# Performance work log

Measured on AMD Instinct MI355X. Metric: run time of the kernel, lower is better.

Reference implementation:

```python
import jax, jax.numpy as jnp
import numpy as np

H = 8          # n_heads
M = 16         # max_dist
U = 512        # n_units
DH = U // H    # d_head
EPS = 1e-3     # keras LayerNormalization default epsilon
NEG = -2.0**32 + 1.0


def _rel_table(pe, T):
    # pe: [2M+1, DH]; returns [T, T, DH] with rel[i, j] = pe[clip(j - i, -M, M) + M]
    i = jnp.arange(T)
    idx = jnp.clip(i[None, :] - i[:, None], -M, M) + M
    return pe[idx]


def _split_heads(x):
    # [B, T, U] -> [H*B, T, DH]  (head-major, matching tf.concat(tf.split(x, H, 2), 0))
    B, T, _ = x.shape
    return x.reshape(B, T, H, DH).transpose(2, 0, 1, 3).reshape(H * B, T, DH)


def _merge_heads(x, B):
    # [H*B, T, DH] -> [B, T, U]
    T = x.shape[1]
    return x.reshape(H, B, T, DH).transpose(1, 2, 0, 3).reshape(B, T, U)


def setup_inputs() -> dict:
    key = jax.random.key(0)
    ks = jax.random.split(key, 10)
    B, T = 8, 1024
    s = 1.0 / np.sqrt(U)
    inp = {
        'q': jax.random.normal(ks[0], (B, T, U), jnp.float32),
        'k': jax.random.normal(ks[1], (B, T, U), jnp.float32),
        'v': jax.random.normal(ks[2], (B, T, U), jnp.float32),
        'Wq': jax.random.normal(ks[3], (U, U), jnp.float32) * s,
        'bq': jnp.zeros((U,), jnp.float32),
        'Wk': jax.random.normal(ks[4], (U, U), jnp.float32) * s,
        'bk': jnp.zeros((U,), jnp.float32),
        'Wv': jax.random.normal(ks[5], (U, U), jnp.float32) * s,
        'bv': jnp.zeros((U,), jnp.float32),
        'Wo': jax.random.normal(ks[6], (U, U), jnp.float32) * s,
        'bo': jnp.zeros((U,), jnp.float32),
        'gamma': jnp.ones((U,), jnp.float32),
        'beta': jnp.zeros((U,), jnp.float32),
        'pe_k': jax.random.normal(ks[7], (2 * M + 1, DH), jnp.float32) * 0.05,
        'pe_v': jax.random.normal(ks[8], (2 * M + 1, DH), jnp.float32) * 0.05,
    }
    return inp


def reference(q, k, v, Wq, bq, Wk, bk, Wv, bv, Wo, bo, gamma, beta, pe_k, pe_v):
    B, T, _ = q.shape
    relu = jax.nn.relu
    q_emb = relu(q @ Wq + bq)
    k_emb = relu(k @ Wk + bk)
    v_emb = relu(v @ Wv + bv)
    qh = _split_heads(q_emb)   # [HB, T, DH]
    kh = _split_heads(k_emb)
    vh = _split_heads(v_emb)

    attn = jnp.einsum('btd,bsd->bts', qh, kh)
    rel_k = _rel_table(pe_k, T)                       # [T, T, DH]
    attn = attn + jnp.einsum('btd,tsd->bts', qh, rel_k)
    attn = attn / jnp.asarray(DH, attn.dtype) ** 0.5

    causal = jnp.tril(jnp.ones((T, T), jnp.bool_))
    attn = jnp.where(causal[None], attn, jnp.asarray(NEG, attn.dtype))
    w = jax.nn.softmax(attn, axis=-1)

    out = jnp.einsum('bts,bsd->btd', w, vh)
    rel_v = _rel_table(pe_v, T)
    out = out + jnp.einsum('bts,tsd->btd', w, rel_v)

    out = _merge_heads(out, B)                        # [B, T, U]
    out = relu(out @ Wo + bo)
    out = out + q

    mu = jnp.mean(out, axis=-1, keepdims=True)
    var = jnp.mean(jnp.square(out - mu), axis=-1, keepdims=True)
    return (out - mu) * jax.lax.rsqrt(var + EPS) * gamma + beta
```

## Files before the change

### kernel.cpp

```cpp
#include <hip/hip_runtime.h>
#include <hip/hip_bf16.h>

#define T_SEQ 1024
#define U_DIM 512
#define LN_EPS 1e-3f

typedef float  f32x4  __attribute__((ext_vector_type(4)));
typedef short  bf16x8 __attribute__((ext_vector_type(8)));

__device__ __forceinline__ unsigned short f2bf(float f) {
    union { float f; unsigned u; } x; x.f = f;
    unsigned r = x.u + 0x7fffu + ((x.u >> 16) & 1u);
    return (unsigned short)(r >> 16);
}
__device__ __forceinline__ float b2f(short s) {
    union { unsigned u; float f; } x; x.u = ((unsigned)(unsigned short)s) << 16;
    return x.f;
}
__device__ __forceinline__ int packbf(float a, float b) {
    return (int)((unsigned)f2bf(a) | ((unsigned)f2bf(b) << 16));
}
__device__ __forceinline__ void async_copy16(void* lds, const void* g) {
    __builtin_amdgcn_global_load_lds((const __attribute__((address_space(1))) void*)g,
                                     (__attribute__((address_space(3))) void*)lds, 16, 0, 0);
}

__global__ __launch_bounds__(256) void prep_wt(
        const float* __restrict__ Wq, const float* __restrict__ Wk,
        const float* __restrict__ Wv, const float* __restrict__ Wo,
        short* __restrict__ wt) {
    __shared__ float Ws[64][65];
    const int bid = blockIdx.x, t = threadIdx.x;
    const int z = bid >> 6, tile = bid & 63;
    const float* W = (z == 0) ? Wq : (z == 1) ? Wk : (z == 2) ? Wv : Wo;
    short* Wt = wt + (size_t)z * 262144;
    const int k0 = (tile >> 3) * 64, n0 = (tile & 7) * 64;
    {
        const int kr = t >> 2, cs = (t & 3) * 16;
        const float4* src = (const float4*)(W + (size_t)(k0 + kr) * 512 + n0 + cs);
#pragma unroll
        for (int i = 0; i < 4; ++i) {
            float4 vv = src[i];
            Ws[kr][cs + 4 * i + 0] = vv.x;
            Ws[kr][cs + 4 * i + 1] = vv.y;
            Ws[kr][cs + 4 * i + 2] = vv.z;
            Ws[kr][cs + 4 * i + 3] = vv.w;
        }
    }
    __syncthreads();
    {
        const int nr = t >> 2, ks = (t & 3) * 16;
        int4 w0, w1;
        w0.x = packbf(Ws[ks + 0][nr], Ws[ks + 1][nr]);
        w0.y = packbf(Ws[ks + 2][nr], Ws[ks + 3][nr]);
        w0.z = packbf(Ws[ks + 4][nr], Ws[ks + 5][nr]);
        w0.w = packbf(Ws[ks + 6][nr], Ws[ks + 7][nr]);
        w1.x = packbf(Ws[ks + 8][nr], Ws[ks + 9][nr]);
        w1.y = packbf(Ws[ks + 10][nr], Ws[ks + 11][nr]);
        w1.z = packbf(Ws[ks + 12][nr], Ws[ks + 13][nr]);
        w1.w = packbf(Ws[ks + 14][nr], Ws[ks + 15][nr]);
        short* dst = Wt + (size_t)(n0 + nr) * 512 + k0 + ks;
        *(int4*)dst = w0;
        *(int4*)(dst + 8) = w1;
    }
}

template <int AFP32, int OUT>
__global__ __launch_bounds__(256) void gemm_mfma(
        const void* __restrict__ A0, const void* __restrict__ A1, const void* __restrict__ A2,
        const short* __restrict__ Wt0, const short* __restrict__ Wt1, const short* __restrict__ Wt2,
        const float* __restrict__ b0p, const float* __restrict__ b1p, const float* __restrict__ b2p,
        const float* __restrict__ resid,
        void* __restrict__ O0, void* __restrict__ O1, void* __restrict__ O2) {
    __shared__ short As[2 * 8192];
    __shared__ short Bs[2 * 8192];

    const int z = blockIdx.z;
    const void* Av = (z == 0) ? A0 : (z == 1) ? A1 : A2;
    const short* Wz = (z == 0) ? Wt0 : (z == 1) ? Wt1 : Wt2;
    const float* bz = (z == 0) ? b0p : (z == 1) ? b1p : b2p;
    void* Ov = (z == 0) ? O0 : (z == 1) ? O1 : O2;

    const int tid = threadIdx.x;
    const int m0 = blockIdx.x * 128, n0 = blockIdx.y * 128;
    const int w = tid >> 6, lane = tid & 63;
    const int n15 = lane & 15, g = lane >> 4;
    const int mh = w >> 1, nh = w & 1;
    const int am = tid >> 1, akh = tid & 1;

    f32x4 acc[4][4];
#pragma unroll
    for (int i = 0; i < 4; ++i)
#pragma unroll
        for (int j = 0; j < 4; ++j) acc[i][j] = (f32x4){0.f, 0.f, 0.f, 0.f};

    float4 areg[8];

#define LOAD_A(CK)                                                                       \
    do {                                                                                 \
        const float* asrc = (const float*)Av + (size_t)(m0 + am) * 512 + (CK) * 64 + akh * 32; \
        _Pragma("unroll")                                                                \
        for (int i = 0; i < 8; ++i) areg[i] = ((const float4*)asrc)[i];                  \
    } while (0)

#define STORE_A(BUF)                                                                     \
    do {                                                                                 \
        short* cell = As + (BUF) * 8192 + (akh * 8 + (am >> 4)) * 512;                   \
        _Pragma("unroll")                                                                \
        for (int gg = 0; gg < 4; ++gg) {                                                 \
            int4 wv;                                                                     \
            wv.x = packbf(areg[2 * gg].x, areg[2 * gg].y);                               \
            wv.y = packbf(areg[2 * gg].z, areg[2 * gg].w);                               \
            wv.z = packbf(areg[2 * gg + 1].x, areg[2 * gg + 1].y);                       \
            wv.w = packbf(areg[2 * gg + 1].z, areg[2 * gg + 1].w);                       \
            *(int4*)(cell + ((am & 15) + 16 * gg) * 8) = wv;                             \
        }                                                                                \
    } while (0)

#define STAGE_B(CK, BUF)                                                                 \
    do {                                                                                 \
        if (w < 2) {                                                                     \
            _Pragma("unroll")                                                            \
            for (int i = 0; i < 8; ++i) {                                                \
                const int kc = i >> 2, nt = w * 4 + (i & 3);                             \
                const short* gp = Wz + (size_t)(n0 + nt * 16 + n15) * 512 + (CK) * 64 + kc * 32 + g * 8; \
                async_copy16(Bs + (BUF) * 8192 + (kc * 8 + nt) * 512, gp);               \
            }                                                                            \
        }                                                                                \
    } while (0)

#define STAGE_A_ASYNC(CK, BUF)                                                           \
    do {                                                                                 \
        if (w >= 2) {                                                                    \
            _Pragma("unroll")                                                            \
            for (int i = 0; i < 8; ++i) {                                                \
                const int kc = i >> 2, mt = (w - 2) * 4 + (i & 3);                       \
                const short* gp = (const short*)Av + (size_t)(m0 + mt * 16 + n15) * 512 + (CK) * 64 + kc * 32 + g * 8; \
                async_copy16(As + (BUF) * 8192 + (kc * 8 + mt) * 512, gp);               \
            }                                                                            \
        }                                                                                \
    } while (0)

    if (AFP32) {
        LOAD_A(0);
        STORE_A(0);
        STAGE_B(0, 0);
        LOAD_A(1);
    } else {
        STAGE_B(0, 0);
        STAGE_A_ASYNC(0, 0);
    }

    for (int ck = 0; ck < 8; ++ck) {
        const int cb = ck & 1, nb = cb ^ 1;
        __syncthreads();
        if (ck < 7) {
            STAGE_B(ck + 1, nb);
            if (!AFP32) STAGE_A_ASYNC(ck + 1, nb);
        }
#pragma unroll
        for (int kc = 0; kc < 2; ++kc) {
            bf16x8 af[4], bfv[4];
#pragma unroll
            for (int i = 0; i < 4; ++i)
                af[i] = *(const bf16x8*)(As + cb * 8192 + (kc * 8 + mh * 4 + i) * 512 + lane * 8);
#pragma unroll
            for (int j = 0; j < 4; ++j)
                bfv[j] = *(const bf16x8*)(Bs + cb * 8192 + (kc * 8 + nh * 4 + j) * 512 + lane * 8);
#pragma unroll
            for (int i = 0; i < 4; ++i)
#pragma unroll
                for (int j = 0; j < 4; ++j)
                    acc[i][j] = __builtin_amdgcn_mfma_f32_16x16x32_bf16(af[i], bfv[j], acc[i][j], 0, 0, 0);
        }
        if (AFP32 && ck < 7) {
            STORE_A(nb);
            if (ck < 6) LOAD_A(ck + 2);
        }
    }
#undef LOAD_A
#undef STORE_A
#undef STAGE_B
#undef STAGE_A_ASYNC

    const int mbase = m0 + mh * 64 + g * 4;
    const int nbase = n0 + nh * 64 + n15;
    const bool even = (n15 & 1) == 0;
    float bj[4];
#pragma unroll
    for (int j = 0; j < 4; ++j) bj[j] = bz[nbase + j * 16];

#pragma unroll
    for (int i = 0; i < 4; ++i) {
        const int mrow = mbase + i * 16;
#pragma unroll
        for (int j = 0; j < 4; ++j) {
            const int ncol = nbase + j * 16;
            f32x4 a = acc[i][j];
            float v0 = fmaxf(a[0] + bj[j], 0.f);
            float v1 = fmaxf(a[1] + bj[j], 0.f);
            float v2 = fmaxf(a[2] + bj[j], 0.f);
            float v3 = fmaxf(a[3] + bj[j], 0.f);
            if (OUT == 0) {
                unsigned t01 = (unsigned)packbf(v0, v1);
                unsigned t23 = (unsigned)packbf(v2, v3);
                unsigned x01 = (unsigned)__shfl_xor((int)t01, 1, 64);
                unsigned x23 = (unsigned)__shfl_xor((int)t23, 1, 64);
                short* Oz = (short*)Ov;
                if (even) {
                    unsigned d0 = (t01 & 0xffffu) | (x01 << 16);
                    unsigned d1 = (t01 >> 16) | (x01 & 0xffff0000u);
                    *(unsigned*)(Oz + (size_t)(mrow + 0) * 512 + ncol) = d0;
                    *(unsigned*)(Oz + (size_t)(mrow + 1) * 512 + ncol) = d1;
                } else {
                    unsigned d2 = (x23 & 0xffffu) | (t23 << 16);
                    unsigned d3 = (x23 >> 16) | (t23 & 0xffff0000u);
                    *(unsigned*)(Oz + (size_t)(mrow + 2) * 512 + ncol - 1) = d2;
                    *(unsigned*)(Oz + (size_t)(mrow + 3) * 512 + ncol - 1) = d3;
                }
            } else {
                float x0 = __shfl_xor(v0, 1, 64);
                float x1 = __shfl_xor(v1, 1, 64);
                float x2 = __shfl_xor(v2, 1, 64);
                float x3 = __shfl_xor(v3, 1, 64);
                float* Oz = (float*)Ov;
                if (even) {
                    float2 r0 = *(const float2*)(resid + (size_t)(mrow + 0) * 512 + ncol);
                    float2 r1 = *(const float2*)(resid + (size_t)(mrow + 1) * 512 + ncol);
                    *(float2*)(Oz + (size_t)(mrow + 0) * 512 + ncol) = make_float2(v0 + r0.x, x0 + r0.y);
                    *(float2*)(Oz + (size_t)(mrow + 1) * 512 + ncol) = make_float2(v1 + r1.x, x1 + r1.y);
                } else {
                    float2 r2 = *(const float2*)(resid + (size_t)(mrow + 2) * 512 + ncol - 1);
                    float2 r3 = *(const float2*)(resid + (size_t)(mrow + 3) * 512 + ncol - 1);
                    *(float2*)(Oz + (size_t)(mrow + 2) * 512 + ncol - 1) = make_float2(x2 + r2.x, v2 + r2.y);
                    *(float2*)(Oz + (size_t)(mrow + 3) * 512 + ncol - 1) = make_float2(x3 + r3.x, v3 + r3.y);
                }
            }
        }
    }
}

__global__ __launch_bounds__(256) void attn_mfma(
        const short* __restrict__ qe, const short* __restrict__ ke,
        const short* __restrict__ ve, const float* __restrict__ pe_k,
        float* __restrict__ ml, short* __restrict__ ao) {
    __shared__ short Kc[2 * 4096];
    __shared__ short Vc[2 * 4096];
    __shared__ float qpeS[4 * 16 * 17];

    const int tid = threadIdx.x;
    const int bx = blockIdx.x;
    const int hb = blockIdx.y;
    const int h = hb >> 3, b = hb & 7;
    const int w = tid >> 6, lane = tid & 63;
    const int g = lane >> 4, n15 = lane & 15;
    const int sp = tid & 31, dbase = (tid >> 5) * 8;
    const int tA = bx;
    float* qpeW = qpeS + w * (16 * 17);

    const size_t rowbase = (size_t)b * T_SEQ;

    int qn = 0;
    bf16x8 Bq[2];
    float qpe0 = 0.f;
    float m_r = -3.0e38f, l_r = 0.f;
    f32x4 oacc[4];

#define SETUP(TILE)                                                                      \
    do {                                                                                 \
        qn = (TILE) * 64 + w * 16;                                                       \
        _Pragma("unroll")                                                                \
        for (int kh = 0; kh < 2; ++kh)                                                   \
            Bq[kh] = *(const bf16x8*)(qe + (rowbase + qn + n15) * U_DIM + h * 64 + kh * 32 + g * 8); \
        f32x4 qa[2];                                                                     \
        qa[0] = (f32x4){0.f, 0.f, 0.f, 0.f};                                             \
        qa[1] = (f32x4){0.f, 0.f, 0.f, 0.f};                                             \
        _Pragma("unroll")                                                                \
        for (int mt = 0; mt < 2; ++mt)                                                   \
        _Pragma("unroll")                                                                \
        for (int kh = 0; kh < 2; ++kh) {                                                 \
            const float* src = pe_k + (mt * 16 + n15) * 64 + kh * 32 + g * 8;            \
            float4 f0 = *(const float4*)src;                                             \
            float4 f1 = *(const float4*)(src + 4);                                       \
            bf16x8 fr;                                                                   \
            fr[0] = (short)f2bf(f0.x); fr[1] = (short)f2bf(f0.y);                        \
            fr[2] = (short)f2bf(f0.z); fr[3] = (short)f2bf(f0.w);                        \
            fr[4] = (short)f2bf(f1.x); fr[5] = (short)f2bf(f1.y);                        \
            fr[6] = (short)f2bf(f1.z); fr[7] = (short)f2bf(f1.w);                        \
            qa[mt] = __builtin_amdgcn_mfma_f32_16x16x32_bf16(fr, Bq[kh], qa[mt], 0, 0, 0); \
        }                                                                                \
        _Pragma("unroll")                                                                \
        for (int mt = 0; mt < 2; ++mt)                                                   \
        _Pragma("unroll")                                                                \
        for (int r = 0; r < 4; ++r) {                                                    \
            const int ri = mt * 16 + 4 * g + r;                                          \
            if (ri <= 16) qpeW[n15 * 17 + ri] = qa[mt][r];                               \
        }                                                                                \
        qpe0 = qpeW[n15 * 17];                                                           \
        m_r = -3.0e38f; l_r = 0.f;                                                       \
        _Pragma("unroll")                                                                \
        for (int dt = 0; dt < 4; ++dt) oacc[dt] = (f32x4){0.f, 0.f, 0.f, 0.f};           \
    } while (0)

#define STAGE_K(S, BUF)                                                                  \
    do {                                                                                 \
        _Pragma("unroll")                                                                \
        for (int j = 0; j < 2; ++j) {                                                    \
            const int cc = w * 2 + j, kh = cc >> 2, mt = cc & 3;                         \
            const short* gp = ke + (rowbase + (S) + mt * 16 + n15) * U_DIM + h * 64 + kh * 32 + g * 8; \
            async_copy16(Kc + (BUF) * 4096 + cc * 512, gp);                              \
        }                                                                                \
    } while (0)

#define LOAD_V(S)                                                                        \
    do {                                                                                 \
        const short* r0 = ve + (rowbase + (S) + 2 * sp) * U_DIM + h * 64 + dbase;        \
        vx = *(const bf16x8*)r0;                                                         \
        vy = *(const bf16x8*)(r0 + U_DIM);                                               \
    } while (0)

#define STORE_V(BUF)                                                                     \
    do {                                                                                 \
        const int vkh = sp >> 4, vg = (sp & 15) >> 2, vj = (sp & 3) * 2;                 \
        _Pragma("unroll")                                                                \
        for (int i = 0; i < 8; ++i) {                                                    \
            const int d = dbase + i;                                                     \
            int pv = (int)((unsigned short)vx[i]) | (((int)(unsigned short)vy[i]) << 16);\
            *(int*)(Vc + (BUF) * 4096 + (vkh * 4 + (d >> 4)) * 512 + ((d & 15) + 16 * vg) * 8 + vj) = pv; \
        }                                                                                \
    } while (0)

    SETUP(tA);
    bf16x8 vx, vy;
    STAGE_K(0, 0);
    LOAD_V(0);
    STORE_V(0);

    for (int gs = 0; gs <= 16; ++gs) {
        const int cb = gs & 1, nb = cb ^ 1;
        const int s0 = (gs <= tA) ? gs * 64 : (gs - tA - 1) * 64;
        __syncthreads();
        if (gs < 16) {
            const int sn = (gs + 1 <= tA) ? (gs + 1) * 64 : (gs - tA) * 64;
            STAGE_K(sn, nb);
            LOAD_V(sn);
        }

        {
            int cls[4];
#pragma unroll
            for (int mt = 0; mt < 4; ++mt) {
                const int slo = s0 + mt * 16;
                cls[mt] = (slo > qn + 15) ? 0 : ((slo + 31 < qn) ? 1 : 2);
            }
            f32x4 c[4];
#pragma unroll
            for (int mt = 0; mt < 4; ++mt) c[mt] = (f32x4){0.f, 0.f, 0.f, 0.f};
#pragma unroll
            for (int mt = 0; mt < 4; ++mt) {
                if (!cls[mt]) continue;
#pragma unroll
                for (int kh = 0; kh < 2; ++kh) {
                    bf16x8 ak = *(const bf16x8*)(Kc + cb * 4096 + (kh * 4 + mt) * 512 + lane * 8);
                    c[mt] = __builtin_amdgcn_mfma_f32_16x16x32_bf16(ak, Bq[kh], c[mt], 0, 0, 0);
                }
            }

            const int qg = qn + n15;
            float sc[4][4];
            float pmax = -3.0e38f;
#pragma unroll
            for (int mt = 0; mt < 4; ++mt) {
                if (cls[mt] == 0) {
#pragma unroll
                    for (int r = 0; r < 4; ++r) sc[mt][r] = -3.0e38f;
                } else if (cls[mt] == 1) {
#pragma unroll
                    for (int r = 0; r < 4; ++r) {
                        sc[mt][r] = (c[mt][r] + qpe0) * 0.125f;
                        pmax = fmaxf(pmax, sc[mt][r]);
                    }
                } else {
#pragma unroll
                    for (int r = 0; r < 4; ++r) {
                        const int sg = s0 + mt * 16 + 4 * g + r;
                        const int dlt = sg - qg;
                        if (dlt <= 0) {
                            const int ri = (dlt < -16) ? 0 : (dlt + 16);
                            sc[mt][r] = (c[mt][r] + qpeW[n15 * 17 + ri]) * 0.125f;
                            pmax = fmaxf(pmax, sc[mt][r]);
                        } else {
                            sc[mt][r] = -3.0e38f;
                        }
                    }
                }
            }
            pmax = fmaxf(pmax, __shfl_xor(pmax, 16, 64));
            pmax = fmaxf(pmax, __shfl_xor(pmax, 32, 64));
            const float mnew = fmaxf(m_r, pmax);
            const float alpha = __expf(m_r - mnew);
            float p[4][4];
            float psum = 0.f;
#pragma unroll
            for (int mt = 0; mt < 4; ++mt)
#pragma unroll
            for (int r = 0; r < 4; ++r) {
                const float pv = (cls[mt] == 0) ? 0.f : __expf(sc[mt][r] - mnew);
                p[mt][r] = pv;
                psum += pv;
            }
            psum += __shfl_xor(psum, 16, 64);
            psum += __shfl_xor(psum, 32, 64);
            l_r = l_r * alpha + psum;
            m_r = mnew;

            int pk01[4], pk23[4];
#pragma unroll
            for (int mt = 0; mt < 4; ++mt) {
                pk01[mt] = packbf(p[mt][0], p[mt][1]);
                pk23[mt] = packbf(p[mt][2], p[mt][3]);
            }
            const int srcA = ((g & 1) * 2) * 16 + n15;
            const int srcB = srcA + 16;
            const bool selHi = (g >> 1) != 0;
            float aO[4];
#pragma unroll
            for (int r = 0; r < 4; ++r) aO[r] = __shfl(alpha, 4 * g + r, 64);
#pragma unroll
            for (int dt = 0; dt < 4; ++dt)
#pragma unroll
            for (int r = 0; r < 4; ++r) oacc[dt][r] *= aO[r];
#pragma unroll
            for (int kh = 0; kh < 2; ++kh) {
                if (cls[2 * kh] == 0 && cls[2 * kh + 1] == 0) continue;
                const int a0l = __shfl(pk01[2 * kh], srcA, 64);
                const int a0h = __shfl(pk01[2 * kh + 1], srcA, 64);
                const int a1l = __shfl(pk23[2 * kh], srcA, 64);
                const int a1h = __shfl(pk23[2 * kh + 1], srcA, 64);
                const int a2l = __shfl(pk01[2 * kh], srcB, 64);
                const int a2h = __shfl(pk01[2 * kh + 1], srcB, 64);
                const int a3l = __shfl(pk23[2 * kh], srcB, 64);
                const int a3h = __shfl(pk23[2 * kh + 1], srcB, 64);
                union { int i[4]; bf16x8 v; } au;
                au.i[0] = selHi ? a0h : a0l;
                au.i[1] = selHi ? a1h : a1l;
                au.i[2] = selHi ? a2h : a2l;
                au.i[3] = selHi ? a3h : a3l;
#pragma unroll
                for (int dt = 0; dt < 4; ++dt) {
                    bf16x8 bv = *(const bf16x8*)(Vc + cb * 4096 + (kh * 4 + dt) * 512 + lane * 8);
                    oacc[dt] = __builtin_amdgcn_mfma_f32_16x16x32_bf16(au.v, bv, oacc[dt], 0, 0, 0);
                }
            }
        }

        if (gs == tA) {
            if (g == 0)
                *(float2*)(ml + ((size_t)hb * T_SEQ + qn + n15) * 2) = make_float2(m_r, l_r);
#pragma unroll
            for (int r = 0; r < 4; ++r) {
                const float lq = __shfl(l_r, 4 * g + r, 64);
                const float linv = 1.0f / lq;
                short* dst = ao + (rowbase + qn + 4 * g + r) * U_DIM + h * 64 + n15;
#pragma unroll
                for (int dt = 0; dt < 4; ++dt)
                    dst[dt * 16] = (short)f2bf(oacc[dt][r] * linv);
            }
            SETUP(15 - bx);
        }

        if (gs < 16) STORE_V(nb);
    }

    if (g == 0)
        *(float2*)(ml + ((size_t)hb * T_SEQ + qn + n15) * 2) = make_float2(m_r, l_r);
#pragma unroll
    for (int r = 0; r < 4; ++r) {
        const float lq = __shfl(l_r, 4 * g + r, 64);
        const float linv = 1.0f / lq;
        short* dst = ao + (rowbase + qn + 4 * g + r) * U_DIM + h * 64 + n15;
#pragma unroll
        for (int dt = 0; dt < 4; ++dt)
            dst[dt * 16] = (short)f2bf(oacc[dt][r] * linv);
    }
#undef SETUP
#undef STAGE_K
#undef LOAD_V
#undef STORE_V
}

__global__ __launch_bounds__(256) void band_relv(
        const short* __restrict__ qe, const short* __restrict__ ke,
        const float* __restrict__ pe_k, const float* __restrict__ pe_v,
        const float* __restrict__ ml, short* __restrict__ ao) {
    __shared__ float pek[17 * 64];
    __shared__ float pev[17 * 64];
    const int tb = blockIdx.x, hb = blockIdx.y;
    const int h = hb >> 3, b = hb & 7;
    const int tid = threadIdx.x;
    for (int i = tid; i < 17 * 64; i += 256) {
        pek[i] = b2f((short)f2bf(pe_k[i]));
        pev[i] = pe_v[i];
    }
    __syncthreads();

    const int t = tb * 64 + (tid >> 2);
    const int p = (tid & 3) * 16;
    const short* qp = qe + (size_t)(b * T_SEQ + t) * U_DIM + h * 64 + p;
    bf16x8 qa = *(const bf16x8*)qp, qb2 = *(const bf16x8*)(qp + 8);
    float qv[16];
#pragma unroll
    for (int i = 0; i < 8; ++i) { qv[i] = b2f(qa[i]); qv[8 + i] = b2f(qb2[i]); }

    float dots[17];
#pragma unroll
    for (int ri = 0; ri < 17; ++ri) {
        const int s = t - 16 + ri;
        float acc = 0.f;
        if (s >= 0) {
            const short* kp = ke + (size_t)(b * T_SEQ + s) * U_DIM + h * 64 + p;
            bf16x8 ka = *(const bf16x8*)kp, kb2 = *(const bf16x8*)(kp + 8);
#pragma unroll
            for (int d = 0; d < 8; ++d) {
                acc += qv[d] * b2f(ka[d]);
                acc += qv[8 + d] * b2f(kb2[d]);
            }
#pragma unroll
            for (int d = 0; d < 16; ++d) acc += qv[d] * pek[ri * 64 + p + d];
        }
        dots[ri] = acc;
    }
#pragma unroll
    for (int ri = 0; ri < 17; ++ri) {
        dots[ri] += __shfl_xor(dots[ri], 1, 64);
        dots[ri] += __shfl_xor(dots[ri], 2, 64);
    }

    const float2 mlv = *(const float2*)(ml + ((size_t)hb * T_SEQ + t) * 2);
    const float m = mlv.x, linv = 1.0f / mlv.y;
    float wv[17];
    float wsum = 0.f;
#pragma unroll
    for (int ri = 0; ri < 17; ++ri) {
        const int s = t - 16 + ri;
        const float wr = (s >= 0) ? __expf(dots[ri] * 0.125f - m) * linv : 0.f;
        wv[ri] = wr;
        wsum += wr;
    }
    wv[0] += 1.0f - wsum;

    float relv[16];
#pragma unroll
    for (int d = 0; d < 16; ++d) relv[d] = 0.f;
#pragma unroll
    for (int ri = 0; ri < 17; ++ri)
#pragma unroll
        for (int d = 0; d < 16; ++d) relv[d] += wv[ri] * pev[ri * 64 + p + d];

    short* op = ao + (size_t)(b * T_SEQ + t) * U_DIM + h * 64 + p;
    bf16x8 a0 = *(const bf16x8*)op, a1 = *(const bf16x8*)(op + 8);
    int4 o0, o1;
    o0.x = packbf(b2f(a0[0]) + relv[0],  b2f(a0[1]) + relv[1]);
    o0.y = packbf(b2f(a0[2]) + relv[2],  b2f(a0[3]) + relv[3]);
    o0.z = packbf(b2f(a0[4]) + relv[4],  b2f(a0[5]) + relv[5]);
    o0.w = packbf(b2f(a0[6]) + relv[6],  b2f(a0[7]) + relv[7]);
    o1.x = packbf(b2f(a1[0]) + relv[8],  b2f(a1[1]) + relv[9]);
    o1.y = packbf(b2f(a1[2]) + relv[10], b2f(a1[3]) + relv[11]);
    o1.z = packbf(b2f(a1[4]) + relv[12], b2f(a1[5]) + relv[13]);
    o1.w = packbf(b2f(a1[6]) + relv[14], b2f(a1[7]) + relv[15]);
    *(int4*)op = o0;
    *(int4*)(op + 8) = o1;
}

__global__ __launch_bounds__(256) void ln_kernel(float* __restrict__ io,
                                                 const float* __restrict__ gamma,
                                                 const float* __restrict__ beta) {
    const int row = blockIdx.x * 4 + (threadIdx.x >> 6);
    const int lane = threadIdx.x & 63;
    float* rp = io + (size_t)row * 512 + lane * 8;
    float4 a = *(const float4*)rp;
    float4 c = *(const float4*)(rp + 4);
    float v[8] = {a.x, a.y, a.z, a.w, c.x, c.y, c.z, c.w};

    float s = v[0] + v[1] + v[2] + v[3] + v[4] + v[5] + v[6] + v[7];
#pragma unroll
    for (int off = 1; off < 64; off <<= 1) s += __shfl_xor(s, off, 64);
    const float mu = s * (1.0f / 512.0f);

    float sq = 0.f;
#pragma unroll
    for (int i = 0; i < 8; ++i) { v[i] -= mu; sq += v[i] * v[i]; }
#pragma unroll
    for (int off = 1; off < 64; off <<= 1) sq += __shfl_xor(sq, off, 64);
    const float rs = rsqrtf(sq * (1.0f / 512.0f) + LN_EPS);

    const float4 g0 = *(const float4*)(gamma + lane * 8);
    const float4 g1 = *(const float4*)(gamma + lane * 8 + 4);
    const float4 b0 = *(const float4*)(beta + lane * 8);
    const float4 b1 = *(const float4*)(beta + lane * 8 + 4);
    float4 o0, o1;
    o0.x = v[0] * rs * g0.x + b0.x;
    o0.y = v[1] * rs * g0.y + b0.y;
    o0.z = v[2] * rs * g0.z + b0.z;
    o0.w = v[3] * rs * g0.w + b0.w;
    o1.x = v[4] * rs * g1.x + b1.x;
    o1.y = v[5] * rs * g1.y + b1.y;
    o1.z = v[6] * rs * g1.z + b1.z;
    o1.w = v[7] * rs * g1.w + b1.w;
    *(float4*)rp = o0;
    *(float4*)(rp + 4) = o1;
}

extern "C" void kernel_launch(void* const* d_in, const int* in_sizes, int n_in,
                              void* d_out, int out_size, void* d_ws, size_t ws_size,
                              hipStream_t stream) {
    const float* q     = (const float*)d_in[0];
    const float* k     = (const float*)d_in[1];
    const float* v     = (const float*)d_in[2];
    const float* Wq    = (const float*)d_in[3];
    const float* bq    = (const float*)d_in[4];
    const float* Wk    = (const float*)d_in[5];
    const float* bk    = (const float*)d_in[6];
    const float* Wv    = (const float*)d_in[7];
    const float* bv    = (const float*)d_in[8];
    const float* Wo    = (const float*)d_in[9];
    const float* bo    = (const float*)d_in[10];
    const float* gamma = (const float*)d_in[11];
    const float* beta  = (const float*)d_in[12];
    const float* pe_k  = (const float*)d_in[13];
    const float* pe_v  = (const float*)d_in[14];
    float* out = (float*)d_out;

    char* base = (char*)d_ws;
    short* qe = (short*)(base);
    short* ke = (short*)(base + (((size_t)8) << 20));
    short* ve = (short*)(base + (((size_t)16) << 20));
    short* ao = (short*)(base + (((size_t)24) << 20));
    short* wt = (short*)(base + (((size_t)32) << 20));
    float* ml = (float*)(base + (((size_t)34) << 20));
    short* wtq = wt, *wtk = wt + 262144, *wtv = wt + 2 * 262144, *wto = wt + 3 * 262144;

    prep_wt<<<dim3(256), 256, 0, stream>>>(Wq, Wk, Wv, Wo, wt);
    gemm_mfma<1, 0><<<dim3(64, 4, 3), 256, 0, stream>>>(
        q, k, v, wtq, wtk, wtv, bq, bk, bv, nullptr, qe, ke, ve);
    attn_mfma<<<dim3(8, 64), 256, 0, stream>>>(qe, ke, ve, pe_k, ml, ao);
    band_relv<<<dim3(16, 64), 256, 0, stream>>>(qe, ke, pe_k, pe_v, ml, ao);
    gemm_mfma<0, 1><<<dim3(64, 4, 1), 256, 0, stream>>>(
        ao, ao, ao, wto, wto, wto, bo, bo, bo, q, out, out, out);
    ln_kernel<<<dim3(2048), 256, 0, stream>>>(out, gamma, beta);
}
```

Measured before the change: 264.3 us.

## Split attention work per query tile, coalesce fp32 A loads, shrink output GEMM tile

After: 240.2 us. 1.1x faster.

```diff
diff --git a/kernel.cpp b/kernel.cpp
--- a/kernel.cpp
+++ b/kernel.cpp
@@ -65,14 +65,18 @@
     }
 }
 
-template <int AFP32, int OUT>
+template <int AFP32, int OUT, int BM>
 __global__ __launch_bounds__(256) void gemm_mfma(
         const void* __restrict__ A0, const void* __restrict__ A1, const void* __restrict__ A2,
         const short* __restrict__ Wt0, const short* __restrict__ Wt1, const short* __restrict__ Wt2,
         const float* __restrict__ b0p, const float* __restrict__ b1p, const float* __restrict__ b2p,
         const float* __restrict__ resid,
         void* __restrict__ O0, void* __restrict__ O1, void* __restrict__ O2) {
-    __shared__ short As[2 * 8192];
+    constexpr int ASZ = BM * 64;
+    constexpr int NW  = (BM == 128) ? 2 : 4;
+    constexpr int AJ  = 8 / NW;
+    constexpr int ACB = BM / 32;
+    __shared__ short As[2 * ASZ];
     __shared__ short Bs[2 * 8192];
 
     const int z = blockIdx.z;
@@ -82,38 +86,37 @@
     void* Ov = (z == 0) ? O0 : (z == 1) ? O1 : O2;
 
     const int tid = threadIdx.x;
-    const int m0 = blockIdx.x * 128, n0 = blockIdx.y * 128;
+    const int m0 = blockIdx.x * BM, n0 = blockIdx.y * 128;
     const int w = tid >> 6, lane = tid & 63;
     const int n15 = lane & 15, g = lane >> 4;
-    const int mh = w >> 1, nh = w & 1;
-    const int am = tid >> 1, akh = tid & 1;
-
-    f32x4 acc[4][4];
+    const int mh = w / NW, nh = w % NW;
+    const int lr = tid >> 4, c4 = tid & 15;
+
+    f32x4 acc[4][AJ];
 #pragma unroll
     for (int i = 0; i < 4; ++i)
 #pragma unroll
-        for (int j = 0; j < 4; ++j) acc[i][j] = (f32x4){0.f, 0.f, 0.f, 0.f};
+        for (int j = 0; j < AJ; ++j) acc[i][j] = (f32x4){0.f, 0.f, 0.f, 0.f};
 
     float4 areg[8];
 
 #define LOAD_A(CK)                                                                       \
     do {                                                                                 \
-        const float* asrc = (const float*)Av + (size_t)(m0 + am) * 512 + (CK) * 64 + akh * 32; \
-        _Pragma("unroll")                                                                \
-        for (int i = 0; i < 8; ++i) areg[i] = ((const float4*)asrc)[i];                  \
+        const float* abase = (const float*)Av + (size_t)(m0 + lr) * 512 + (CK) * 64 + c4 * 4; \
+        _Pragma("unroll")                                                                \
+        for (int i = 0; i < 8; ++i) areg[i] = *(const float4*)(abase + (size_t)8192 * i); \
     } while (0)
 
 #define STORE_A(BUF)                                                                     \
     do {                                                                                 \
-        short* cell = As + (BUF) * 8192 + (akh * 8 + (am >> 4)) * 512;                   \
-        _Pragma("unroll")                                                                \
-        for (int gg = 0; gg < 4; ++gg) {                                                 \
-            int4 wv;                                                                     \
-            wv.x = packbf(areg[2 * gg].x, areg[2 * gg].y);                               \
-            wv.y = packbf(areg[2 * gg].z, areg[2 * gg].w);                               \
-            wv.z = packbf(areg[2 * gg + 1].x, areg[2 * gg + 1].y);                       \
-            wv.w = packbf(areg[2 * gg + 1].z, areg[2 * gg + 1].w);                       \
-            *(int4*)(cell + ((am & 15) + 16 * gg) * 8) = wv;                             \
+        short* sb = As + (BUF) * ASZ + ((c4 >> 3) * (BM / 16)) * 512 + lr * 8 +          \
+                    ((c4 & 7) >> 1) * 128 + (c4 & 1) * 4;                                \
+        _Pragma("unroll")                                                                \
+        for (int i = 0; i < 8; ++i) {                                                    \
+            int2 wv;                                                                     \
+            wv.x = packbf(areg[i].x, areg[i].y);                                         \
+            wv.y = packbf(areg[i].z, areg[i].w);                                         \
+            *(int2*)(sb + i * 512) = wv;                                                 \
         }                                                                                \
     } while (0)
 
@@ -133,10 +136,10 @@
     do {                                                                                 \
         if (w >= 2) {                                                                    \
             _Pragma("unroll")                                                            \
-            for (int i = 0; i < 8; ++i) {                                                \
-                const int kc = i >> 2, mt = (w - 2) * 4 + (i & 3);                       \
+            for (int i = 0; i < 2 * ACB; ++i) {                                          \
+                const int kc = i / ACB, mt = (w - 2) * ACB + (i % ACB);                  \
                 const short* gp = (const short*)Av + (size_t)(m0 + mt * 16 + n15) * 512 + (CK) * 64 + kc * 32 + g * 8; \
-                async_copy16(As + (BUF) * 8192 + (kc * 8 + mt) * 512, gp);               \
+                async_copy16(As + (BUF) * ASZ + (kc * (BM / 16) + mt) * 512, gp);        \
             }                                                                            \
         }                                                                                \
     } while (0)
@@ -160,17 +163,17 @@
         }
 #pragma unroll
         for (int kc = 0; kc < 2; ++kc) {
-            bf16x8 af[4], bfv[4];
+            bf16x8 af[4], bfv[AJ];
 #pragma unroll
             for (int i = 0; i < 4; ++i)
-                af[i] = *(const bf16x8*)(As + cb * 8192 + (kc * 8 + mh * 4 + i) * 512 + lane * 8);
-#pragma unroll
-            for (int j = 0; j < 4; ++j)
-                bfv[j] = *(const bf16x8*)(Bs + cb * 8192 + (kc * 8 + nh * 4 + j) * 512 + lane * 8);
+                af[i] = *(const bf16x8*)(As + cb * ASZ + (kc * (BM / 16) + mh * 4 + i) * 512 + lane * 8);
+#pragma unroll
+            for (int j = 0; j < AJ; ++j)
+                bfv[j] = *(const bf16x8*)(Bs + cb * 8192 + (kc * 8 + nh * AJ + j) * 512 + lane * 8);
 #pragma unroll
             for (int i = 0; i < 4; ++i)
 #pragma unroll
-                for (int j = 0; j < 4; ++j)
+                for (int j = 0; j < AJ; ++j)
                     acc[i][j] = __builtin_amdgcn_mfma_f32_16x16x32_bf16(af[i], bfv[j], acc[i][j], 0, 0, 0);
         }
         if (AFP32 && ck < 7) {
@@ -184,17 +187,17 @@
 #undef STAGE_A_ASYNC
 
     const int mbase = m0 + mh * 64 + g * 4;
-    const int nbase = n0 + nh * 64 + n15;
+    const int nbase = n0 + nh * (AJ * 16) + n15;
     const bool even = (n15 & 1) == 0;
-    float bj[4];
-#pragma unroll
-    for (int j = 0; j < 4; ++j) bj[j] = bz[nbase + j * 16];
+    float bj[AJ];
+#pragma unroll
+    for (int j = 0; j < AJ; ++j) bj[j] = bz[nbase + j * 16];
 
 #pragma unroll
     for (int i = 0; i < 4; ++i) {
         const int mrow = mbase + i * 16;
 #pragma unroll
-        for (int j = 0; j < 4; ++j) {
+        for (int j = 0; j < AJ; ++j) {
             const int ncol = nbase + j * 16;
             f32x4 a = acc[i][j];
             float v0 = fmaxf(a[0] + bj[j], 0.f);
@@ -249,13 +252,14 @@
     __shared__ float qpeS[4 * 16 * 17];
 
     const int tid = threadIdx.x;
-    const int bx = blockIdx.x;
-    const int hb = blockIdx.y;
+    const int bid = blockIdx.x;
+    const int rank = (bid & 3) + 4 * (bid >> 8);
+    const int hb = (bid >> 2) & 63;
+    const int tt = 15 - rank;
     const int h = hb >> 3, b = hb & 7;
     const int w = tid >> 6, lane = tid & 63;
     const int g = lane >> 4, n15 = lane & 15;
     const int sp = tid & 31, dbase = (tid >> 5) * 8;
-    const int tA = bx;
     float* qpeW = qpeS + w * (16 * 17);
 
     const size_t rowbase = (size_t)b * T_SEQ;
@@ -330,20 +334,19 @@
         }                                                                                \
     } while (0)
 
-    SETUP(tA);
+    SETUP(tt);
     bf16x8 vx, vy;
     STAGE_K(0, 0);
     LOAD_V(0);
     STORE_V(0);
 
-    for (int gs = 0; gs <= 16; ++gs) {
+    for (int gs = 0; gs <= tt; ++gs) {
         const int cb = gs & 1, nb = cb ^ 1;
-        const int s0 = (gs <= tA) ? gs * 64 : (gs - tA - 1) * 64;
+        const int s0 = gs * 64;
         __syncthreads();
-        if (gs < 16) {
-            const int sn = (gs + 1 <= tA) ? (gs + 1) * 64 : (gs - tA) * 64;
-            STAGE_K(sn, nb);
-            LOAD_V(sn);
+        if (gs < tt) {
+            STAGE_K((gs + 1) * 64, nb);
+            LOAD_V((gs + 1) * 64);
         }
 
         {
@@ -454,22 +457,7 @@
             }
         }
 
-        if (gs == tA) {
-            if (g == 0)
-                *(float2*)(ml + ((size_t)hb * T_SEQ + qn + n15) * 2) = make_float2(m_r, l_r);
-#pragma unroll
-            for (int r = 0; r < 4; ++r) {
-                const float lq = __shfl(l_r, 4 * g + r, 64);
-                const float linv = 1.0f / lq;
-                short* dst = ao + (rowbase + qn + 4 * g + r) * U_DIM + h * 64 + n15;
-#pragma unroll
-                for (int dt = 0; dt < 4; ++dt)
-                    dst[dt * 16] = (short)f2bf(oacc[dt][r] * linv);
-            }
-            SETUP(15 - bx);
-        }
-
-        if (gs < 16) STORE_V(nb);
+        if (gs < tt) STORE_V(nb);
     }
 
     if (g == 0)
@@ -641,11 +629,11 @@
     short* wtq = wt, *wtk = wt + 262144, *wtv = wt + 2 * 262144, *wto = wt + 3 * 262144;
 
     prep_wt<<<dim3(256), 256, 0, stream>>>(Wq, Wk, Wv, Wo, wt);
-    gemm_mfma<1, 0><<<dim3(64, 4, 3), 256, 0, stream>>>(
+    gemm_mfma<1, 0, 128><<<dim3(64, 4, 3), 256, 0, stream>>>(
         q, k, v, wtq, wtk, wtv, bq, bk, bv, nullptr, qe, ke, ve);
-    attn_mfma<<<dim3(8, 64), 256, 0, stream>>>(qe, ke, ve, pe_k, ml, ao);
+    attn_mfma<<<dim3(1024), 256, 0, stream>>>(qe, ke, ve, pe_k, ml, ao);
     band_relv<<<dim3(16, 64), 256, 0, stream>>>(qe, ke, pe_k, pe_v, ml, ao);
-    gemm_mfma<0, 1><<<dim3(64, 4, 1), 256, 0, stream>>>(
+    gemm_mfma<0, 1, 64><<<dim3(128, 4, 1), 256, 0, stream>>>(
         ao, ao, ao, wto, wto, wto, bo, bo, bo, q, out, out, out);
     ln_kernel<<<dim3(2048), 256, 0, stream>>>(out, gamma, beta);
 }
```
